# Kernel tuning notes

Hardware: AMD Instinct MI355X
Metric: run time of the kernel (lower is better)

## Reference

```python
import jax, jax.numpy as jnp
import numpy as np

C = 512
NUM_HEADS = 8


def setup_inputs() -> dict:
    key = jax.random.key(0)
    ks = jax.random.split(key, 9)
    s = 1.0 / np.sqrt(C)
    inp = {
        "x": jax.random.normal(ks[0], (2, C, 64, 64), dtype=jnp.float32),
        "Wq": jax.random.uniform(ks[1], (C, C), jnp.float32, -s, s),
        "bq": jax.random.uniform(ks[2], (C,), jnp.float32, -s, s),
        "Wk": jax.random.uniform(ks[3], (C, C), jnp.float32, -s, s),
        "bk": jax.random.uniform(ks[4], (C,), jnp.float32, -s, s),
        "Wv": jax.random.uniform(ks[5], (C, C), jnp.float32, -s, s),
        "bv": jax.random.uniform(ks[6], (C,), jnp.float32, -s, s),
        "Wp": jax.random.uniform(ks[7], (C, C), jnp.float32, -s, s),
        "bp": jax.random.uniform(ks[8], (C,), jnp.float32, -s, s),
    }
    return inp


def _split_heads(t):
    # [B, S, C] -> [B, h, S, d]
    B, S, Ct = t.shape
    return t.reshape(B, S, NUM_HEADS, Ct // NUM_HEADS).transpose(0, 2, 1, 3)


def reference(x, Wq, bq, Wk, bk, Wv, bv, Wp, bp):
    B, Ct, H, W = x.shape
    tok = x.transpose(0, 2, 3, 1).reshape(B, H * W, Ct)  # [B, S, C]
    q = _split_heads(tok @ Wq.T + bq)
    k = _split_heads(tok @ Wk.T + bk)
    v = _split_heads(tok @ Wv.T + bv)
    d = q.shape[-1]
    scores = jnp.einsum("bhsd,bhtd->bhst", q, k) / jnp.sqrt(jnp.float32(d))
    attn = jax.nn.softmax(scores, axis=-1)
    out = jnp.einsum("bhst,bhtd->bhsd", attn, v)
    out = out.transpose(0, 2, 1, 3).reshape(B, H * W, Ct)  # merge heads
    out = out @ Wp.T + bp
    return out.reshape(B, H, W, Ct).transpose(0, 3, 1, 2)
```

## Files before the change

### kernel.cpp

```cpp
#include <hip/hip_runtime.h>
#include <stdint.h>
#include <math.h>

typedef unsigned short u16;
typedef uint32_t u32;
typedef short bf16x8 __attribute__((ext_vector_type(8)));
typedef float f32x4  __attribute__((ext_vector_type(4)));

#define DEV __device__ __forceinline__

DEV u16 f2bf(float f) {
    union { float f; u32 u; } x; x.f = f;
    u32 lsb = (x.u >> 16) & 1u;
    x.u += 0x7fffu + lsb;
    return (u16)(x.u >> 16);
}

DEV u32 pack2(float a, float b) {
    union { float f; u32 u; } x, y; x.f = a; y.f = b;
    return __builtin_amdgcn_perm(y.u + 0x8000u, x.u + 0x8000u, 0x07060302u);
}

#if __has_builtin(__builtin_amdgcn_exp2f)
DEV float fexp2(float x) { return __builtin_amdgcn_exp2f(x); }
#else
DEV float fexp2(float x) { return __expf(x * 0.69314718056f); }
#endif

DEV f32x4 mfma16(bf16x8 a, bf16x8 b, f32x4 c) {
    return __builtin_amdgcn_mfma_f32_16x16x32_bf16(a, b, c, 0, 0, 0);
}

__global__ __launch_bounds__(256) void convert_w_kernel(const float* __restrict__ w0,
                                                        const float* __restrict__ w1,
                                                        const float* __restrict__ w2,
                                                        const float* __restrict__ w3,
                                                        u16* __restrict__ dst) {
    const float* src = (blockIdx.y == 0) ? w0 : (blockIdx.y == 1) ? w1
                     : (blockIdx.y == 2) ? w2 : w3;
    int idx = (blockIdx.x * 256 + threadIdx.x) * 4;
    float4 v = *(const float4*)&src[idx];
    uint2 pv;
    pv.x = pack2(v.x, v.y);
    pv.y = pack2(v.z, v.w);
    *(uint2*)&dst[(size_t)blockIdx.y * 262144 + idx] = pv;
}

__global__ __launch_bounds__(256) void transpose_kernel(const float* __restrict__ x,
                                                        u16* __restrict__ tok) {
    __shared__ u16 t[64][65];
    const int b = blockIdx.z, c0 = blockIdx.y * 64, s0 = blockIdx.x * 64;
    const float* xb = x + ((size_t)b * 512 + c0) * 4096 + s0;
    u16* tb = tok + ((size_t)b * 4096 + s0) * 512 + c0;
    const int tid = threadIdx.x;
    {
        const int jc = tid & 15, i0 = tid >> 4;
#pragma unroll
        for (int ii = 0; ii < 4; ii++) {
            int i = i0 * 4 + ii;
            float4 v = *(const float4*)&xb[(size_t)i * 4096 + jc * 4];
            t[i][jc * 4 + 0] = f2bf(v.x);
            t[i][jc * 4 + 1] = f2bf(v.y);
            t[i][jc * 4 + 2] = f2bf(v.z);
            t[i][jc * 4 + 3] = f2bf(v.w);
        }
    }
    __syncthreads();
    {
        const int j = tid & 31, i0 = tid >> 5;
#pragma unroll
        for (int ii = 0; ii < 8; ii++) {
            int srow = i0 * 8 + ii;
            u32 v = (u32)t[j * 2][srow] | ((u32)t[j * 2 + 1][srow] << 16);
            *(u32*)(&tb[(size_t)srow * 512 + j * 2]) = v;
        }
    }
}

DEV void proj_core(const u16* __restrict__ W, const float* __restrict__ bias,
                   const u16* __restrict__ Bb, void* __restrict__ out,
                   int b, int mode, float scale,
                   u16* __restrict__ Alds, u16* __restrict__ Blds) {
    const int tid = threadIdx.x;
    const int wave = tid >> 6, lane = tid & 63, q = lane >> 4, c = lane & 15;
    const int m0 = blockIdx.y * 64, n0 = blockIdx.x * 128;

    f32x4 acc[4][2] = {};

    for (int k0 = 0; k0 < 512; k0 += 64) {
        __syncthreads();
#pragma unroll
        for (int i = 0; i < 2; i++) {
            int g = tid + i * 256;
            int r = g & 15, qq = (g >> 4) & 3, ks = (g >> 6) & 1, rt = g >> 7;
            int col = k0 + ks * 32 + qq * 8;
            *(int4*)&Alds[g * 8] = *(const int4*)&W[(size_t)(m0 + rt * 16 + r) * 512 + col];
        }
#pragma unroll
        for (int i = 0; i < 4; i++) {
            int g = tid + i * 256;
            int r = g & 15, qq = (g >> 4) & 3, ks = (g >> 6) & 1, rt = g >> 7;
            int col = k0 + ks * 32 + qq * 8;
            *(int4*)&Blds[g * 8] = *(const int4*)&Bb[(size_t)(n0 + rt * 16 + r) * 512 + col];
        }
        __syncthreads();
#pragma unroll
        for (int ks = 0; ks < 2; ks++) {
            bf16x8 af[4], bfr[2];
#pragma unroll
            for (int mt = 0; mt < 4; mt++)
                af[mt] = *(const bf16x8*)&Alds[(((mt * 2 + ks) * 4 + q) * 16 + c) * 8];
#pragma unroll
            for (int nt = 0; nt < 2; nt++) {
                int ntg = wave * 2 + nt;
                bfr[nt] = *(const bf16x8*)&Blds[(((ntg * 2 + ks) * 4 + q) * 16 + c) * 8];
            }
#pragma unroll
            for (int mt = 0; mt < 4; mt++)
#pragma unroll
                for (int nt = 0; nt < 2; nt++)
                    acc[mt][nt] = mfma16(af[mt], bfr[nt], acc[mt][nt]);
        }
    }

#pragma unroll
    for (int mt = 0; mt < 4; mt++) {
        int co0 = m0 + mt * 16 + q * 4;
        float b0 = bias[co0 + 0], b1 = bias[co0 + 1];
        float b2 = bias[co0 + 2], b3 = bias[co0 + 3];
#pragma unroll
        for (int nt = 0; nt < 2; nt++) {
            int scol = n0 + wave * 32 + nt * 16 + c;
            float v0 = (acc[mt][nt][0] + b0) * scale;
            float v1 = (acc[mt][nt][1] + b1) * scale;
            float v2 = (acc[mt][nt][2] + b2) * scale;
            float v3 = (acc[mt][nt][3] + b3) * scale;
            if (mode == 0) {
                uint2 pv; pv.x = pack2(v0, v1); pv.y = pack2(v2, v3);
                size_t idx = ((size_t)(b * 8 + (co0 >> 6)) * 4096 + scol) * 64 + (co0 & 63);
                *(uint2*)&((u16*)out)[idx] = pv;
            } else if (mode == 1) {
                u16* o = (u16*)out;
                o[((size_t)(b * 512 + co0 + 0)) * 4096 + scol] = f2bf(v0);
                o[((size_t)(b * 512 + co0 + 1)) * 4096 + scol] = f2bf(v1);
                o[((size_t)(b * 512 + co0 + 2)) * 4096 + scol] = f2bf(v2);
                o[((size_t)(b * 512 + co0 + 3)) * 4096 + scol] = f2bf(v3);
            } else {
                float* o = (float*)out;
                o[((size_t)(b * 512 + co0 + 0)) * 4096 + scol] = v0;
                o[((size_t)(b * 512 + co0 + 1)) * 4096 + scol] = v1;
                o[((size_t)(b * 512 + co0 + 2)) * 4096 + scol] = v2;
                o[((size_t)(b * 512 + co0 + 3)) * 4096 + scol] = v3;
            }
        }
    }
}

__global__ __launch_bounds__(256) void qkv_kernel(const u16* __restrict__ Wbf,
                                                  const float* __restrict__ bq,
                                                  const float* __restrict__ bk,
                                                  const float* __restrict__ bv,
                                                  const u16* __restrict__ tok,
                                                  u16* __restrict__ Qb,
                                                  u16* __restrict__ Kb,
                                                  u16* __restrict__ Vb) {
    __shared__ u16 Alds[4096];
    __shared__ u16 Blds[8192];
    const int z = blockIdx.z, j = z >> 1, b = z & 1;
    const u16* W = Wbf + (size_t)j * 262144;
    const float* bias = (j == 0) ? bq : (j == 1) ? bk : bv;
    void* out = (j == 0) ? (void*)Qb : (j == 1) ? (void*)Kb : (void*)Vb;
    const float scale = (j == 0) ? 0.1803368801f : 1.0f;
    const int mode = (j == 2) ? 1 : 0;
    proj_core(W, bias, tok + (size_t)b * (4096 * 512), out, b, mode, scale, Alds, Blds);
}

__global__ __launch_bounds__(256) void projp_kernel(const u16* __restrict__ Wp,
                                                    const float* __restrict__ bp,
                                                    const u16* __restrict__ attout,
                                                    float* __restrict__ out) {
    __shared__ u16 Alds[4096];
    __shared__ u16 Blds[8192];
    const int b = blockIdx.z;
    proj_core(Wp, bp, attout + (size_t)b * (4096 * 512), out, b, 2, 1.0f, Alds, Blds);
}

__global__ __launch_bounds__(256) void attn_kernel(const u16* __restrict__ Qm,
                                                   const u16* __restrict__ Km,
                                                   const u16* __restrict__ Vm,
                                                   u16* __restrict__ attout) {
    __shared__ u16 Klds[2][4096];
    __shared__ u16 Vlds[2][4096];
    __shared__ u16 Plds[128 * 72];
    const int tid = threadIdx.x, wave = tid >> 6, lane = tid & 63;
    const int q = lane >> 4, c = lane & 15;
    const int bhd = blockIdx.y, s0 = blockIdx.x * 128;
    const u16* Qb = Qm + (size_t)bhd * (4096 * 64);
    const u16* Kb = Km + (size_t)bhd * (4096 * 64);
    const u16* Vb = Vm + (size_t)bhd * (64 * 4096);

    bf16x8 qf[2][2];
#pragma unroll
    for (int st = 0; st < 2; st++)
#pragma unroll
        for (int kd = 0; kd < 2; kd++)
            qf[st][kd] = *(const bf16x8*)
                &Qb[(size_t)(s0 + wave * 32 + st * 16 + c) * 64 + kd * 32 + q * 8];

    const int rr = tid & 15, qq = (tid >> 4) & 3, kk = (tid >> 6) & 1;
    const int t40 = tid >> 7, t41 = t40 + 2;
    const u16* Ksrc0 = Kb + (size_t)(t40 * 16 + rr) * 64 + kk * 32 + qq * 8;
    const u16* Ksrc1 = Kb + (size_t)(t41 * 16 + rr) * 64 + kk * 32 + qq * 8;
    const u16* Vsrc0 = Vb + (size_t)(t40 * 16 + rr) * 4096 + kk * 32 + qq * 8;
    const u16* Vsrc1 = Vb + (size_t)(t41 * 16 + rr) * 4096 + kk * 32 + qq * 8;
    u16* Prow = &Plds[(size_t)(wave * 32 + c) * 72];

    f32x4 oacc[4][2] = {};
    float lsum[2] = {0.f, 0.f};

    *(int4*)&Klds[0][tid * 8]         = *(const int4*)&Ksrc0[0];
    *(int4*)&Klds[0][(tid + 256) * 8] = *(const int4*)&Ksrc1[0];
    *(int4*)&Vlds[0][tid * 8]         = *(const int4*)&Vsrc0[0];
    *(int4*)&Vlds[0][(tid + 256) * 8] = *(const int4*)&Vsrc1[0];
    __syncthreads();

    for (int it = 0; it < 64; it++) {
        const int p = it & 1;
        const size_t t0n = (size_t)(((it + 1) & 63) * 64);

        int4 kst0 = *(const int4*)&Ksrc0[t0n * 64];
        int4 kst1 = *(const int4*)&Ksrc1[t0n * 64];
        int4 vst0 = *(const int4*)&Vsrc0[t0n];
        int4 vst1 = *(const int4*)&Vsrc1[t0n];

        f32x4 sacc[4][2] = {};
#pragma unroll
        for (int kd = 0; kd < 2; kd++) {
            bf16x8 ka[4];
#pragma unroll
            for (int tt = 0; tt < 4; tt++)
                ka[tt] = *(const bf16x8*)&Klds[p][(((tt * 2 + kd) * 4 + q) * 16 + c) * 8];
#pragma unroll
            for (int tt = 0; tt < 4; tt++)
#pragma unroll
                for (int st = 0; st < 2; st++)
                    sacc[tt][st] = mfma16(ka[tt], qf[st][kd], sacc[tt][st]);
        }

#pragma unroll
        for (int st = 0; st < 2; st++) {
#pragma unroll
            for (int tt = 0; tt < 4; tt++) {
                float p0 = fexp2(sacc[tt][st][0]);
                float p1 = fexp2(sacc[tt][st][1]);
                float p2 = fexp2(sacc[tt][st][2]);
                float p3 = fexp2(sacc[tt][st][3]);
                lsum[st] += (p0 + p1) + (p2 + p3);
                uint2 pv; pv.x = pack2(p0, p1); pv.y = pack2(p2, p3);
                *(uint2*)&Prow[st * (16 * 72) + tt * 16 + q * 4] = pv;
            }
        }

#pragma unroll
        for (int kt = 0; kt < 2; kt++) {
            bf16x8 va[4], pb[2];
#pragma unroll
            for (int dt = 0; dt < 4; dt++)
                va[dt] = *(const bf16x8*)&Vlds[p][(((dt * 2 + kt) * 4 + q) * 16 + c) * 8];
#pragma unroll
            for (int st = 0; st < 2; st++)
                pb[st] = *(const bf16x8*)&Prow[st * (16 * 72) + kt * 32 + q * 8];
#pragma unroll
            for (int dt = 0; dt < 4; dt++)
#pragma unroll
                for (int st = 0; st < 2; st++)
                    oacc[dt][st] = mfma16(va[kt == 0 ? dt : dt], pb[st], oacc[dt][st]);
        }

        *(int4*)&Klds[1 - p][tid * 8]         = kst0;
        *(int4*)&Klds[1 - p][(tid + 256) * 8] = kst1;
        *(int4*)&Vlds[1 - p][tid * 8]         = vst0;
        *(int4*)&Vlds[1 - p][(tid + 256) * 8] = vst1;
        __syncthreads();
    }

    const int b = bhd >> 3, hd = bhd & 7;
#pragma unroll
    for (int st = 0; st < 2; st++) {
        float l = lsum[st];
        l += __shfl_xor(l, 16, 64);
        l += __shfl_xor(l, 32, 64);
        float rl = 1.0f / l;
        int s = s0 + wave * 32 + st * 16 + c;
#pragma unroll
        for (int dt = 0; dt < 4; dt++) {
            uint2 pv;
            pv.x = pack2(oacc[dt][st][0] * rl, oacc[dt][st][1] * rl);
            pv.y = pack2(oacc[dt][st][2] * rl, oacc[dt][st][3] * rl);
            size_t idx = ((size_t)(b * 4096 + s)) * 512 + hd * 64 + dt * 16 + q * 4;
            *(uint2*)&attout[idx] = pv;
        }
    }
}

extern "C" void kernel_launch(void* const* d_in, const int* in_sizes, int n_in,
                              void* d_out, int out_size, void* d_ws, size_t ws_size,
                              hipStream_t stream) {
    (void)in_sizes; (void)n_in; (void)out_size; (void)ws_size;
    const float* x  = (const float*)d_in[0];
    const float* Wq = (const float*)d_in[1];
    const float* bq = (const float*)d_in[2];
    const float* Wk = (const float*)d_in[3];
    const float* bk = (const float*)d_in[4];
    const float* Wv = (const float*)d_in[5];
    const float* bv = (const float*)d_in[6];
    const float* Wp = (const float*)d_in[7];
    const float* bp = (const float*)d_in[8];
    float* out = (float*)d_out;

    const size_t NTOK = (size_t)4 * 1024 * 1024;
    u16* tok = (u16*)d_ws;
    u16* Qb  = tok + NTOK;
    u16* Kb  = Qb + NTOK;
    u16* Vb  = Kb + NTOK;
    u16* Wbf = Vb + NTOK;
    u16* attout = tok;

    convert_w_kernel<<<dim3(256, 4), 256, 0, stream>>>(Wq, Wk, Wv, Wp, Wbf);
    transpose_kernel<<<dim3(64, 8, 2), 256, 0, stream>>>(x, tok);
    qkv_kernel<<<dim3(32, 8, 6), 256, 0, stream>>>(Wbf, bq, bk, bv, tok, Qb, Kb, Vb);
    attn_kernel<<<dim3(32, 16), 256, 0, stream>>>(Qb, Kb, Vb, attout);
    projp_kernel<<<dim3(32, 8, 2), 256, 0, stream>>>(Wbf + 3 * 262144, bp, attout, out);
}
```

Before: 242.8 us.

## Double-buffer projection GEMM LDS and enlarge tile to 128x128

```diff
diff --git a/kernel.cpp b/kernel.cpp
--- a/kernel.cpp
+++ b/kernel.cpp
@@ -80,57 +80,64 @@
 DEV void proj_core(const u16* __restrict__ W, const float* __restrict__ bias,
                    const u16* __restrict__ Bb, void* __restrict__ out,
                    int b, int mode, float scale,
-                   u16* __restrict__ Alds, u16* __restrict__ Blds) {
+                   u16 (*__restrict__ Alds)[4096], u16 (*__restrict__ Blds)[4096]) {
     const int tid = threadIdx.x;
     const int wave = tid >> 6, lane = tid & 63, q = lane >> 4, c = lane & 15;
-    const int m0 = blockIdx.y * 64, n0 = blockIdx.x * 128;
-
-    f32x4 acc[4][2] = {};
-
-    for (int k0 = 0; k0 < 512; k0 += 64) {
+    const int m0 = blockIdx.y * 128, n0 = blockIdx.x * 128;
+
+    const int cs = tid & 15, qs = (tid >> 4) & 3, ms = (tid >> 6) & 3;
+    const u16* Asrc0 = W  + (size_t)(m0 + ms * 16 + cs) * 512 + qs * 8;
+    const u16* Asrc1 = W  + (size_t)(m0 + (ms + 4) * 16 + cs) * 512 + qs * 8;
+    const u16* Bsrc0 = Bb + (size_t)(n0 + ms * 16 + cs) * 512 + qs * 8;
+    const u16* Bsrc1 = Bb + (size_t)(n0 + (ms + 4) * 16 + cs) * 512 + qs * 8;
+
+    f32x4 acc[4][4] = {};
+
+    *(int4*)&Alds[0][tid * 8]         = *(const int4*)&Asrc0[0];
+    *(int4*)&Alds[0][(tid + 256) * 8] = *(const int4*)&Asrc1[0];
+    *(int4*)&Blds[0][tid * 8]         = *(const int4*)&Bsrc0[0];
+    *(int4*)&Blds[0][(tid + 256) * 8] = *(const int4*)&Bsrc1[0];
+    __syncthreads();
+
+    for (int it = 0; it < 16; it++) {
+        const int p = it & 1;
+        const int kn = ((it + 1) & 15) * 32;
+
+        int4 ast0 = *(const int4*)&Asrc0[kn];
+        int4 ast1 = *(const int4*)&Asrc1[kn];
+        int4 bst0 = *(const int4*)&Bsrc0[kn];
+        int4 bst1 = *(const int4*)&Bsrc1[kn];
+
+        bf16x8 af[4], bfr[4];
+#pragma unroll
+        for (int t = 0; t < 4; t++) {
+            int gm = (((wave & 1) * 4 + t) * 4 + q) * 16 + c;
+            af[t] = *(const bf16x8*)&Alds[p][gm * 8];
+            int gn = (((wave >> 1) * 4 + t) * 4 + q) * 16 + c;
+            bfr[t] = *(const bf16x8*)&Blds[p][gn * 8];
+        }
+#pragma unroll
+        for (int mt = 0; mt < 4; mt++)
+#pragma unroll
+            for (int nt = 0; nt < 4; nt++)
+                acc[mt][nt] = mfma16(af[mt], bfr[nt], acc[mt][nt]);
+
+        *(int4*)&Alds[1 - p][tid * 8]         = ast0;
+        *(int4*)&Alds[1 - p][(tid + 256) * 8] = ast1;
+        *(int4*)&Blds[1 - p][tid * 8]         = bst0;
+        *(int4*)&Blds[1 - p][(tid + 256) * 8] = bst1;
         __syncthreads();
-#pragma unroll
-        for (int i = 0; i < 2; i++) {
-            int g = tid + i * 256;
-            int r = g & 15, qq = (g >> 4) & 3, ks = (g >> 6) & 1, rt = g >> 7;
-            int col = k0 + ks * 32 + qq * 8;
-            *(int4*)&Alds[g * 8] = *(const int4*)&W[(size_t)(m0 + rt * 16 + r) * 512 + col];
-        }
-#pragma unroll
-        for (int i = 0; i < 4; i++) {
-            int g = tid + i * 256;
-            int r = g & 15, qq = (g >> 4) & 3, ks = (g >> 6) & 1, rt = g >> 7;
-            int col = k0 + ks * 32 + qq * 8;
-            *(int4*)&Blds[g * 8] = *(const int4*)&Bb[(size_t)(n0 + rt * 16 + r) * 512 + col];
-        }
-        __syncthreads();
-#pragma unroll
-        for (int ks = 0; ks < 2; ks++) {
-            bf16x8 af[4], bfr[2];
-#pragma unroll
-            for (int mt = 0; mt < 4; mt++)
-                af[mt] = *(const bf16x8*)&Alds[(((mt * 2 + ks) * 4 + q) * 16 + c) * 8];
-#pragma unroll
-            for (int nt = 0; nt < 2; nt++) {
-                int ntg = wave * 2 + nt;
-                bfr[nt] = *(const bf16x8*)&Blds[(((ntg * 2 + ks) * 4 + q) * 16 + c) * 8];
-            }
-#pragma unroll
-            for (int mt = 0; mt < 4; mt++)
-#pragma unroll
-                for (int nt = 0; nt < 2; nt++)
-                    acc[mt][nt] = mfma16(af[mt], bfr[nt], acc[mt][nt]);
-        }
-    }
-
+    }
+
+    const int mbase = m0 + (wave & 1) * 64, nbase = n0 + (wave >> 1) * 64;
 #pragma unroll
     for (int mt = 0; mt < 4; mt++) {
-        int co0 = m0 + mt * 16 + q * 4;
+        int co0 = mbase + mt * 16 + q * 4;
         float b0 = bias[co0 + 0], b1 = bias[co0 + 1];
         float b2 = bias[co0 + 2], b3 = bias[co0 + 3];
 #pragma unroll
-        for (int nt = 0; nt < 2; nt++) {
-            int scol = n0 + wave * 32 + nt * 16 + c;
+        for (int nt = 0; nt < 4; nt++) {
+            int scol = nbase + nt * 16 + c;
             float v0 = (acc[mt][nt][0] + b0) * scale;
             float v1 = (acc[mt][nt][1] + b1) * scale;
             float v2 = (acc[mt][nt][2] + b2) * scale;
@@ -164,8 +171,8 @@
                                                   u16* __restrict__ Qb,
                                                   u16* __restrict__ Kb,
                                                   u16* __restrict__ Vb) {
-    __shared__ u16 Alds[4096];
-    __shared__ u16 Blds[8192];
+    __shared__ u16 Alds[2][4096];
+    __shared__ u16 Blds[2][4096];
     const int z = blockIdx.z, j = z >> 1, b = z & 1;
     const u16* W = Wbf + (size_t)j * 262144;
     const float* bias = (j == 0) ? bq : (j == 1) ? bk : bv;
@@ -179,8 +186,8 @@
                                                     const float* __restrict__ bp,
                                                     const u16* __restrict__ attout,
                                                     float* __restrict__ out) {
-    __shared__ u16 Alds[4096];
-    __shared__ u16 Blds[8192];
+    __shared__ u16 Alds[2][4096];
+    __shared__ u16 Blds[2][4096];
     const int b = blockIdx.z;
     proj_core(Wp, bp, attout + (size_t)b * (4096 * 512), out, b, 2, 1.0f, Alds, Blds);
 }
@@ -274,7 +281,7 @@
             for (int dt = 0; dt < 4; dt++)
 #pragma unroll
                 for (int st = 0; st < 2; st++)
-                    oacc[dt][st] = mfma16(va[kt == 0 ? dt : dt], pb[st], oacc[dt][st]);
+                    oacc[dt][st] = mfma16(va[dt], pb[st], oacc[dt][st]);
         }
 
         *(int4*)&Klds[1 - p][tid * 8]         = kst0;
@@ -328,7 +335,7 @@
 
     convert_w_kernel<<<dim3(256, 4), 256, 0, stream>>>(Wq, Wk, Wv, Wp, Wbf);
     transpose_kernel<<<dim3(64, 8, 2), 256, 0, stream>>>(x, tok);
-    qkv_kernel<<<dim3(32, 8, 6), 256, 0, stream>>>(Wbf, bq, bk, bv, tok, Qb, Kb, Vb);
+    qkv_kernel<<<dim3(32, 4, 6), 256, 0, stream>>>(Wbf, bq, bk, bv, tok, Qb, Kb, Vb);
     attn_kernel<<<dim3(32, 16), 256, 0, stream>>>(Qb, Kb, Vb, attout);
-    projp_kernel<<<dim3(32, 8, 2), 256, 0, stream>>>(Wbf + 3 * 262144, bp, attout, out);
-}
+    projp_kernel<<<dim3(32, 4, 2), 256, 0, stream>>>(Wbf + 3 * 262144, bp, attout, out);
+}
```

Result: faster. 232.9 us (-4.0%).
